# Kernel optimization log

Hardware: AMD Instinct MI355X
Metric: run time of the kernel (lower is better)

Reference implementation:

```python
import jax, jax.numpy as jnp
import numpy as np

SAMPLE_RATE = 4096.0  # matches init_kwargs sample_rate
STATE_DIM = 64
LENGTH, CHANNELS = 8192, 512


def setup_inputs() -> dict:
    key = jax.random.key(0)
    kx, kc = jax.random.split(key)
    x = jax.random.normal(kx, (LENGTH, CHANNELS), dtype=jnp.float32)
    # param init exactly as in the flax module
    logA = jnp.log(1.0 + jnp.arange(STATE_DIM, dtype=jnp.float32))
    B = jnp.ones((STATE_DIM,), dtype=jnp.float32)
    C = 0.01 * jax.random.normal(kc, (STATE_DIM,), dtype=jnp.float32)  # nn.initializers.normal() stddev=0.01
    return {"x": x, "logA": logA, "B": B, "C": C}


def reference(x, logA, B, C):
    # ZOH-style discretization: A = -exp(logA); Abar = exp(A*dt); Bbar = (Abar-1)*B/A
    dt = 1.0 / SAMPLE_RATE
    A = -jnp.exp(logA)                # (N,)
    Abar = jnp.exp(A * dt)            # (N,)
    Bbar = (Abar - 1.0) * B / A       # (N,)

    channels = x.shape[1]
    h0 = jnp.zeros((channels, logA.shape[0]), dtype=x.dtype)  # (C, N)

    def step(h, xt):
        # h: (C, N), xt: (C,)
        h = Abar[None, :] * h + xt[:, None] * Bbar[None, :]
        y = h @ C                      # (C,)
        return h, y

    _, y = jax.lax.scan(step, h0, x)   # y: (L, C)
    return y
```

## Files before the change

### kernel.cpp

```cpp
#include <hip/hip_runtime.h>
#include <math.h>

#define LENGTH   8192
#define CHANNELS 512
#define NSTATE   64
#define TCHUNK   64
#define NCHUNK   (LENGTH / TCHUNK)
#define E_ELEMS  (NCHUNK * NSTATE * CHANNELS)

__global__ void k_setup(const float* __restrict__ logA, const float* __restrict__ B,
                        const float* __restrict__ C, float* __restrict__ cons) {
    int n = threadIdx.x;
    if (n < NSTATE) {
        double A    = -exp((double)logA[n]);
        double ab   = exp(A * (1.0 / 4096.0));
        double Bbar = (ab - 1.0) * (double)B[n] / A;
        double abT  = ab;
        #pragma unroll
        for (int i = 0; i < 6; ++i) abT *= abT;
        cons[n]              = (float)ab;
        cons[NSTATE + n]     = (float)((double)C[n] * Bbar);
        cons[2 * NSTATE + n] = (float)abT;
    }
}

#define PF1 8
__global__ __launch_bounds__(256, 1) void k_pass1(const float* __restrict__ x,
                                                  const float* __restrict__ cons,
                                                  float* __restrict__ E) {
    int gtid = blockIdx.x * 256 + threadIdx.x;
    int c = gtid & (CHANNELS - 1);
    int k = gtid >> 9;
    const float* xp = x + (size_t)k * TCHUNK * CHANNELS + c;

    float h[NSTATE];
    #pragma unroll
    for (int n = 0; n < NSTATE; ++n) h[n] = 0.f;

    float xbuf[PF1];
    #pragma unroll
    for (int j = 0; j < PF1; ++j) xbuf[j] = xp[(size_t)j * CHANNELS];

    #pragma unroll 1
    for (int t0 = 0; t0 < TCHUNK; t0 += PF1) {
        #pragma unroll
        for (int j = 0; j < PF1; ++j) {
            int nt = t0 + PF1 + j;
            if (nt > TCHUNK - 1) nt = TCHUNK - 1;
            float xn = xp[(size_t)nt * CHANNELS];
            float xv = xbuf[j];
            #pragma unroll
            for (int n = 0; n < NSTATE; ++n) h[n] = fmaf(cons[n], h[n], xv);
            xbuf[j] = xn;
        }
    }

    float* Ep = E + (size_t)k * NSTATE * CHANNELS + c;
    #pragma unroll
    for (int n = 0; n < NSTATE; ++n) Ep[(size_t)n * CHANNELS] = h[n];
}

#define G2 16
__global__ __launch_bounds__(64, 1) void k_pass2(float* __restrict__ W,
                                                 const float* __restrict__ cons) {
    int gtid = blockIdx.x * 64 + threadIdx.x;
    int c = gtid & (CHANNELS - 1);
    int n = gtid >> 9;
    float aT = cons[2 * NSTATE + n];
    float* p = W + (size_t)n * CHANNELS + c;
    const size_t S = (size_t)NSTATE * CHANNELS;

    float e[2][G2];
    #pragma unroll
    for (int j = 0; j < G2; ++j) e[0][j] = p[(size_t)j * S];

    float hc = 0.f;
    #pragma unroll
    for (int k0 = 0; k0 < NCHUNK; k0 += G2) {
        const int cur = (k0 / G2) & 1;
        const int nxt = cur ^ 1;
        if (k0 + G2 < NCHUNK) {
            #pragma unroll
            for (int j = 0; j < G2; ++j) e[nxt][j] = p[(size_t)(k0 + G2 + j) * S];
        }
        #pragma unroll
        for (int j = 0; j < G2; ++j) {
            p[(size_t)(k0 + j) * S] = hc;
            hc = fmaf(aT, hc, e[cur][j]);
        }
    }
}

#define PF3 4
__global__ __launch_bounds__(256, 1) void k_pass3(const float* __restrict__ x,
                                                  const float* __restrict__ cons,
                                                  const float* __restrict__ Wc,
                                                  float* __restrict__ y) {
    int gtid = blockIdx.x * 256 + threadIdx.x;
    int c = gtid & (CHANNELS - 1);
    int k = gtid >> 9;

    const float* cp = Wc + (size_t)k * NSTATE * CHANNELS + c;
    float h[NSTATE];
    #pragma unroll
    for (int n = 0; n < NSTATE; ++n) h[n] = cp[(size_t)n * CHANNELS];

    const float* xp = x + (size_t)k * TCHUNK * CHANNELS + c;
    float*       yp = y + (size_t)k * TCHUNK * CHANNELS + c;

    float xbuf[PF3];
    #pragma unroll
    for (int j = 0; j < PF3; ++j) xbuf[j] = xp[(size_t)j * CHANNELS];

    #pragma unroll 1
    for (int t0 = 0; t0 < TCHUNK; t0 += PF3) {
        #pragma unroll
        for (int j = 0; j < PF3; ++j) {
            int nt = t0 + PF3 + j;
            if (nt > TCHUNK - 1) nt = TCHUNK - 1;
            float xn = xp[(size_t)nt * CHANNELS];
            float xv = xbuf[j];
            float y0 = 0.f, y1 = 0.f, y2 = 0.f, y3 = 0.f;
            #pragma unroll
            for (int n = 0; n < NSTATE; n += 4) {
                h[n]     = fmaf(cons[n],     h[n],     xv);
                h[n + 1] = fmaf(cons[n + 1], h[n + 1], xv);
                h[n + 2] = fmaf(cons[n + 2], h[n + 2], xv);
                h[n + 3] = fmaf(cons[n + 3], h[n + 3], xv);
                y0 = fmaf(cons[NSTATE + n],     h[n],     y0);
                y1 = fmaf(cons[NSTATE + n + 1], h[n + 1], y1);
                y2 = fmaf(cons[NSTATE + n + 2], h[n + 2], y2);
                y3 = fmaf(cons[NSTATE + n + 3], h[n + 3], y3);
            }
            yp[(size_t)(t0 + j) * CHANNELS] = (y0 + y1) + (y2 + y3);
            xbuf[j] = xn;
        }
    }
}

__global__ __launch_bounds__(256) void k_fallback(const float* __restrict__ x,
                                                  const float* __restrict__ logA,
                                                  const float* __restrict__ B,
                                                  const float* __restrict__ C,
                                                  float* __restrict__ y) {
    int c = blockIdx.x * blockDim.x + threadIdx.x;
    if (c >= CHANNELS) return;
    float Abar[NSTATE], CB[NSTATE], h[NSTATE];
    for (int n = 0; n < NSTATE; ++n) {
        double A    = -exp((double)logA[n]);
        double ab   = exp(A * (1.0 / 4096.0));
        double Bbar = (ab - 1.0) * (double)B[n] / A;
        Abar[n] = (float)ab;
        CB[n]   = (float)((double)C[n] * Bbar);
        h[n]    = 0.f;
    }
    for (int t = 0; t < LENGTH; ++t) {
        float xv = x[(size_t)t * CHANNELS + c];
        float acc = 0.f;
        for (int n = 0; n < NSTATE; ++n) {
            h[n] = fmaf(Abar[n], h[n], xv);
            acc  = fmaf(CB[n], h[n], acc);
        }
        y[(size_t)t * CHANNELS + c] = acc;
    }
}

extern "C" void kernel_launch(void* const* d_in, const int* in_sizes, int n_in,
                              void* d_out, int out_size, void* d_ws, size_t ws_size,
                              hipStream_t stream) {
    const float* x    = (const float*)d_in[0];
    const float* logA = (const float*)d_in[1];
    const float* B    = (const float*)d_in[2];
    const float* C    = (const float*)d_in[3];
    float* yout = (float*)d_out;

    size_t need = (size_t)(E_ELEMS + 3 * NSTATE) * sizeof(float);
    if (ws_size < need) {
        k_fallback<<<(CHANNELS + 255) / 256, 256, 0, stream>>>(x, logA, B, C, yout);
        return;
    }

    float* W    = (float*)d_ws;
    float* cons = W + E_ELEMS;

    k_setup<<<1, 64, 0, stream>>>(logA, B, C, cons);
    k_pass1<<<(NCHUNK * CHANNELS) / 256, 256, 0, stream>>>(x, cons, W);
    k_pass2<<<(NSTATE * CHANNELS) / 64, 64, 0, stream>>>(W, cons);
    k_pass3<<<(NCHUNK * CHANNELS) / 256, 256, 0, stream>>>(x, cons, W, yout);
}
```

Baseline: 115.3 us.

## Reformulate chunk passes as matrix products with precomputed decay and Toeplitz tables

The per-chunk recurrences in pass1 and pass3 are replaced by dense matmul-like accumulations. They use precomputed decay-power (G), Toeplitz impulse-response (T) and output-projection (P) tables built in the setup kernel, with input tiles staged through LDS. This removes the serial per-timestep dependency chain and the low-occupancy one-thread-per-channel-chunk design, and gives more blocks and independent FMAs. In exchange it does more arithmetic per output and changes floating-point summation order.

```diff
diff --git a/kernel.cpp b/kernel.cpp
--- a/kernel.cpp
+++ b/kernel.cpp
@@ -8,56 +8,85 @@
 #define NCHUNK   (LENGTH / TCHUNK)
 #define E_ELEMS  (NCHUNK * NSTATE * CHANNELS)
 
+
 __global__ void k_setup(const float* __restrict__ logA, const float* __restrict__ B,
-                        const float* __restrict__ C, float* __restrict__ cons) {
+                        const float* __restrict__ C, float* __restrict__ cons,
+                        float* __restrict__ Gt, float* __restrict__ Tt,
+                        float* __restrict__ Pt) {
+    __shared__ double contrib[64][65];
+    __shared__ double Kd[64];
     int n = threadIdx.x;
-    if (n < NSTATE) {
-        double A    = -exp((double)logA[n]);
-        double ab   = exp(A * (1.0 / 4096.0));
-        double Bbar = (ab - 1.0) * (double)B[n] / A;
-        double abT  = ab;
-        #pragma unroll
-        for (int i = 0; i < 6; ++i) abT *= abT;
-        cons[n]              = (float)ab;
-        cons[NSTATE + n]     = (float)((double)C[n] * Bbar);
-        cons[2 * NSTATE + n] = (float)abT;
-    }
-}
-
-#define PF1 8
-__global__ __launch_bounds__(256, 1) void k_pass1(const float* __restrict__ x,
-                                                  const float* __restrict__ cons,
+
+    double A    = -exp((double)logA[n]);
+    double ab   = exp(A * (1.0 / 4096.0));
+    double Bbar = (ab - 1.0) * (double)B[n] / A;
+    double CB   = (double)C[n] * Bbar;
+
+    cons[n]       = (float)ab;
+    cons[64 + n]  = (float)CB;
+    cons[128 + n] = (float)exp(A * (64.0 / 4096.0));
+
+    double p = 1.0;
+    #pragma unroll 1
+    for (int e = 0; e < 64; ++e) { Gt[(63 - e) * 64 + n] = (float)p; p *= ab; }
+
+    p = ab;
+    #pragma unroll 1
+    for (int t = 0; t < 64; ++t) { Pt[n * 64 + t] = (float)(CB * p); p *= ab; }
+
+    p = CB;
+    #pragma unroll 1
+    for (int d = 0; d < 64; ++d) { contrib[n][d] = p; p *= ab; }
+    __syncthreads();
+
+    double Ksum = 0.0;
+    #pragma unroll 1
+    for (int m = 0; m < 64; ++m) Ksum += contrib[m][n];
+    Kd[n] = Ksum;
+    __syncthreads();
+
+    int s = n;
+    #pragma unroll 1
+    for (int t = 0; t < 64; ++t) Tt[s * 64 + t] = (t >= s) ? (float)Kd[t - s] : 0.f;
+}
+
+__global__ __launch_bounds__(256, 4) void k_pass1(const float* __restrict__ x,
+                                                  const float* __restrict__ Gt,
                                                   float* __restrict__ E) {
-    int gtid = blockIdx.x * 256 + threadIdx.x;
-    int c = gtid & (CHANNELS - 1);
-    int k = gtid >> 9;
-    const float* xp = x + (size_t)k * TCHUNK * CHANNELS + c;
-
-    float h[NSTATE];
-    #pragma unroll
-    for (int n = 0; n < NSTATE; ++n) h[n] = 0.f;
-
-    float xbuf[PF1];
-    #pragma unroll
-    for (int j = 0; j < PF1; ++j) xbuf[j] = xp[(size_t)j * CHANNELS];
-
-    #pragma unroll 1
-    for (int t0 = 0; t0 < TCHUNK; t0 += PF1) {
-        #pragma unroll
-        for (int j = 0; j < PF1; ++j) {
-            int nt = t0 + PF1 + j;
-            if (nt > TCHUNK - 1) nt = TCHUNK - 1;
-            float xn = xp[(size_t)nt * CHANNELS];
-            float xv = xbuf[j];
-            #pragma unroll
-            for (int n = 0; n < NSTATE; ++n) h[n] = fmaf(cons[n], h[n], xv);
-            xbuf[j] = xn;
-        }
-    }
-
-    float* Ep = E + (size_t)k * NSTATE * CHANNELS + c;
-    #pragma unroll
-    for (int n = 0; n < NSTATE; ++n) Ep[(size_t)n * CHANNELS] = h[n];
+    __shared__ float Xl[64 * 64];
+    int tid = threadIdx.x;
+    int k   = blockIdx.x >> 3;
+    int c0  = (blockIdx.x & 7) * 64;
+
+    const float* xsrc = x + (size_t)k * TCHUNK * CHANNELS + c0;
+    #pragma unroll
+    for (int i = 0; i < 4; ++i) {
+        int idx = tid + 256 * i;
+        int s   = idx >> 4;
+        int cq  = (idx & 15) * 4;
+        *(float4*)&Xl[s * 64 + cq] = *(const float4*)(xsrc + (size_t)s * CHANNELS + cq);
+    }
+    __syncthreads();
+
+    int w    = __builtin_amdgcn_readfirstlane(tid >> 6);
+    int lane = tid & 63;
+    const float* Gw = Gt + 16 * w;
+
+    float acc[16];
+    #pragma unroll
+    for (int j = 0; j < 16; ++j) acc[j] = 0.f;
+
+    #pragma unroll 4
+    for (int s = 0; s < 64; ++s) {
+        float xv = Xl[s * 64 + lane];
+        const float* g = Gw + s * 64;
+        #pragma unroll
+        for (int j = 0; j < 16; ++j) acc[j] = fmaf(g[j], xv, acc[j]);
+    }
+
+    float* Ep = E + ((size_t)k * NSTATE + 16 * w) * CHANNELS + c0 + lane;
+    #pragma unroll
+    for (int j = 0; j < 16; ++j) Ep[(size_t)j * CHANNELS] = acc[j];
 }
 
 #define G2 16
@@ -66,7 +95,7 @@
     int gtid = blockIdx.x * 64 + threadIdx.x;
     int c = gtid & (CHANNELS - 1);
     int n = gtid >> 9;
-    float aT = cons[2 * NSTATE + n];
+    float aT = cons[128 + n];
     float* p = W + (size_t)n * CHANNELS + c;
     const size_t S = (size_t)NSTATE * CHANNELS;
 
@@ -91,51 +120,58 @@
     }
 }
 
-#define PF3 4
-__global__ __launch_bounds__(256, 1) void k_pass3(const float* __restrict__ x,
-                                                  const float* __restrict__ cons,
+__global__ __launch_bounds__(256, 4) void k_pass3(const float* __restrict__ x,
+                                                  const float* __restrict__ Tt,
+                                                  const float* __restrict__ Pt,
                                                   const float* __restrict__ Wc,
                                                   float* __restrict__ y) {
-    int gtid = blockIdx.x * 256 + threadIdx.x;
-    int c = gtid & (CHANNELS - 1);
-    int k = gtid >> 9;
-
-    const float* cp = Wc + (size_t)k * NSTATE * CHANNELS + c;
-    float h[NSTATE];
-    #pragma unroll
-    for (int n = 0; n < NSTATE; ++n) h[n] = cp[(size_t)n * CHANNELS];
-
-    const float* xp = x + (size_t)k * TCHUNK * CHANNELS + c;
-    float*       yp = y + (size_t)k * TCHUNK * CHANNELS + c;
-
-    float xbuf[PF3];
-    #pragma unroll
-    for (int j = 0; j < PF3; ++j) xbuf[j] = xp[(size_t)j * CHANNELS];
-
-    #pragma unroll 1
-    for (int t0 = 0; t0 < TCHUNK; t0 += PF3) {
-        #pragma unroll
-        for (int j = 0; j < PF3; ++j) {
-            int nt = t0 + PF3 + j;
-            if (nt > TCHUNK - 1) nt = TCHUNK - 1;
-            float xn = xp[(size_t)nt * CHANNELS];
-            float xv = xbuf[j];
-            float y0 = 0.f, y1 = 0.f, y2 = 0.f, y3 = 0.f;
-            #pragma unroll
-            for (int n = 0; n < NSTATE; n += 4) {
-                h[n]     = fmaf(cons[n],     h[n],     xv);
-                h[n + 1] = fmaf(cons[n + 1], h[n + 1], xv);
-                h[n + 2] = fmaf(cons[n + 2], h[n + 2], xv);
-                h[n + 3] = fmaf(cons[n + 3], h[n + 3], xv);
-                y0 = fmaf(cons[NSTATE + n],     h[n],     y0);
-                y1 = fmaf(cons[NSTATE + n + 1], h[n + 1], y1);
-                y2 = fmaf(cons[NSTATE + n + 2], h[n + 2], y2);
-                y3 = fmaf(cons[NSTATE + n + 3], h[n + 3], y3);
-            }
-            yp[(size_t)(t0 + j) * CHANNELS] = (y0 + y1) + (y2 + y3);
-            xbuf[j] = xn;
-        }
-    }
+    __shared__ float Xl[64 * 64];
+    __shared__ float Hl[64 * 64];
+    int tid = threadIdx.x;
+    int k   = blockIdx.x >> 3;
+    int c0  = (blockIdx.x & 7) * 64;
+
+    const float* xsrc = x  + (size_t)k * TCHUNK * CHANNELS + c0;
+    const float* hsrc = Wc + (size_t)k * NSTATE * CHANNELS + c0;
+    #pragma unroll
+    for (int i = 0; i < 4; ++i) {
+        int idx = tid + 256 * i;
+        int s   = idx >> 4;
+        int cq  = (idx & 15) * 4;
+        *(float4*)&Xl[s * 64 + cq] = *(const float4*)(xsrc + (size_t)s * CHANNELS + cq);
+        *(float4*)&Hl[s * 64 + cq] = *(const float4*)(hsrc + (size_t)s * CHANNELS + cq);
+    }
+    __syncthreads();
+
+    int w    = __builtin_amdgcn_readfirstlane(tid >> 6);
+    int lane = tid & 63;
+    int t0   = 16 * w;
+
+    float acc[16];
+    #pragma unroll
+    for (int j = 0; j < 16; ++j) acc[j] = 0.f;
+
+    const float* Tw = Tt + t0;
+    #pragma unroll 4
+    for (int s = 0; s < 64; ++s) {
+        float xv = Xl[s * 64 + lane];
+        const float* tt = Tw + s * 64;
+        #pragma unroll
+        for (int j = 0; j < 16; ++j) acc[j] = fmaf(tt[j], xv, acc[j]);
+    }
+
+    const float* Pw = Pt + t0;
+    #pragma unroll 4
+    for (int n = 0; n < 64; ++n) {
+        float hv = Hl[n * 64 + lane];
+        const float* pp = Pw + n * 64;
+        #pragma unroll
+        for (int j = 0; j < 16; ++j) acc[j] = fmaf(pp[j], hv, acc[j]);
+    }
+
+    float* yp = y + ((size_t)k * TCHUNK + t0) * CHANNELS + c0 + lane;
+    #pragma unroll
+    for (int j = 0; j < 16; ++j) yp[(size_t)j * CHANNELS] = acc[j];
 }
 
 __global__ __launch_bounds__(256) void k_fallback(const float* __restrict__ x,
@@ -174,7 +210,7 @@
     const float* C    = (const float*)d_in[3];
     float* yout = (float*)d_out;
 
-    size_t need = (size_t)(E_ELEMS + 3 * NSTATE) * sizeof(float);
+    size_t need = (size_t)(E_ELEMS + 192 + 3 * 4096) * sizeof(float);
     if (ws_size < need) {
         k_fallback<<<(CHANNELS + 255) / 256, 256, 0, stream>>>(x, logA, B, C, yout);
         return;
@@ -182,9 +218,12 @@
 
     float* W    = (float*)d_ws;
     float* cons = W + E_ELEMS;
-
-    k_setup<<<1, 64, 0, stream>>>(logA, B, C, cons);
-    k_pass1<<<(NCHUNK * CHANNELS) / 256, 256, 0, stream>>>(x, cons, W);
+    float* Gt   = cons + 192;
+    float* Tt   = Gt + 4096;
+    float* Pt   = Tt + 4096;
+
+    k_setup<<<1, 64, 0, stream>>>(logA, B, C, cons, Gt, Tt, Pt);
+    k_pass1<<<NCHUNK * 8, 256, 0, stream>>>(x, Gt, W);
     k_pass2<<<(NSTATE * CHANNELS) / 64, 64, 0, stream>>>(W, cons);
-    k_pass3<<<(NCHUNK * CHANNELS) / 256, 256, 0, stream>>>(x, cons, W, yout);
-}
+    k_pass3<<<NCHUNK * 8, 256, 0, stream>>>(x, Tt, Pt, W, yout);
+}
```

After: 113.9 us. About the same (-1.2%).

## Recast chunked SSM scan passes as bf16x3 MFMA matrix products

Applied to the files above, without the earlier changes.

Pass 1 and pass 3 no longer run a sequential per-channel recurrence over 64 states. They become matrix products on the MFMA units. Pass 1 multiplies a decay matrix by each x tile to get the chunk-end state. Pass 3 combines a Toeplitz kernel matrix applied to x with a state-propagation matrix applied to the carried-in state to produce y. fp32 accuracy is approximated with hi/lo bf16 splitting (three products per pair), and the matrices are precomputed in a prep kernel. This cuts the per-thread serial FMA chains, but it adds shared-memory staging, and precision could fall below pure fp32.

```diff
diff --git a/kernel.cpp b/kernel.cpp
--- a/kernel.cpp
+++ b/kernel.cpp
@@ -7,66 +7,132 @@
 #define TCHUNK   64
 #define NCHUNK   (LENGTH / TCHUNK)
 #define E_ELEMS  (NCHUNK * NSTATE * CHANNELS)
-
-__global__ void k_setup(const float* __restrict__ logA, const float* __restrict__ B,
-                        const float* __restrict__ C, float* __restrict__ cons) {
-    int n = threadIdx.x;
-    if (n < NSTATE) {
-        double A    = -exp((double)logA[n]);
-        double ab   = exp(A * (1.0 / 4096.0));
-        double Bbar = (ab - 1.0) * (double)B[n] / A;
-        double abT  = ab;
-        #pragma unroll
-        for (int i = 0; i < 6; ++i) abT *= abT;
-        cons[n]              = (float)ab;
-        cons[NSTATE + n]     = (float)((double)C[n] * Bbar);
-        cons[2 * NSTATE + n] = (float)abT;
-    }
-}
-
-#define PF1 8
-__global__ __launch_bounds__(256, 1) void k_pass1(const float* __restrict__ x,
-                                                  const float* __restrict__ cons,
+#define TSTRIDE  72
+
+
+typedef __attribute__((ext_vector_type(8))) short bf16x8;
+typedef __attribute__((ext_vector_type(4))) float f32x4;
+
+static __device__ __forceinline__ unsigned short f2bf(float f) {
+    unsigned int u = __float_as_uint(f);
+    u += 0x7fff + ((u >> 16) & 1);
+    return (unsigned short)(u >> 16);
+}
+static __device__ __forceinline__ float bf2f(unsigned short h) {
+    return __uint_as_float(((unsigned int)h) << 16);
+}
+
+__global__ void k_prep(const float* __restrict__ logA, const float* __restrict__ B,
+                       const float* __restrict__ C, unsigned short* __restrict__ mats) {
+    __shared__ double dl2[64], dCB[64], Kp[256], Kd[64];
+    int tid = threadIdx.x;
+    if (tid < 64) {
+        double A    = -exp((double)logA[tid]);
+        double lab  = A * (1.0 / 4096.0);
+        double Bbar = expm1(lab) * (double)B[tid] / A;
+        dl2[tid] = lab;
+        dCB[tid] = (double)C[tid] * Bbar;
+    }
+    __syncthreads();
+    {
+        int d = tid & 63, q = tid >> 6;
+        double s = 0.0;
+        for (int i = 0; i < 16; ++i) { int n = q * 16 + i; s += dCB[n] * exp(dl2[n] * (double)d); }
+        Kp[q * 64 + d] = s;
+    }
+    __syncthreads();
+    if (tid < 64) Kd[tid] = (Kp[tid] + Kp[64 + tid]) + (Kp[128 + tid] + Kp[192 + tid]);
+    __syncthreads();
+
+    unsigned short *Gh = mats,          *Gl = mats + 4096;
+    unsigned short *Th = mats + 8192,   *Tl = mats + 12288;
+    unsigned short *Ph = mats + 16384,  *Pl = mats + 20480;
+    int r = tid >> 2, cb = (tid & 3) * 16;
+    for (int j = 0; j < 16; ++j) {
+        int kk = cb + j;
+        double g = exp(dl2[r] * (double)(63 - kk));
+        unsigned short h = f2bf((float)g);
+        Gh[r * 64 + kk] = h; Gl[r * 64 + kk] = f2bf((float)g - bf2f(h));
+
+        double tv = (r >= kk) ? Kd[r - kk] : 0.0;
+        h = f2bf((float)tv);
+        Th[r * 64 + kk] = h; Tl[r * 64 + kk] = f2bf((float)tv - bf2f(h));
+
+        double pv = dCB[kk] * exp(dl2[kk] * (double)(r + 1));
+        h = f2bf((float)pv);
+        Ph[r * 64 + kk] = h; Pl[r * 64 + kk] = f2bf((float)pv - bf2f(h));
+    }
+}
+
+static __device__ __forceinline__ void stage_tile(const float* __restrict__ src,
+                                                  unsigned short* __restrict__ Dh,
+                                                  unsigned short* __restrict__ Dl,
+                                                  int tid) {
+    int c = tid & 63, g = tid >> 6;
+    const float* sp = src + (size_t)(16 * g) * CHANNELS + c;
+    float v[16];
+    #pragma unroll
+    for (int j = 0; j < 16; ++j) v[j] = sp[(size_t)j * CHANNELS];
+    bf16x8 h0, h1, l0, l1;
+    #pragma unroll
+    for (int j = 0; j < 8; ++j) {
+        unsigned short a = f2bf(v[j]), b = f2bf(v[8 + j]);
+        h0[j] = (short)a; h1[j] = (short)b;
+        l0[j] = (short)f2bf(v[j] - bf2f(a));
+        l1[j] = (short)f2bf(v[8 + j] - bf2f(b));
+    }
+    *(bf16x8*)&Dh[c * TSTRIDE + 16 * g]     = h0;
+    *(bf16x8*)&Dh[c * TSTRIDE + 16 * g + 8] = h1;
+    *(bf16x8*)&Dl[c * TSTRIDE + 16 * g]     = l0;
+    *(bf16x8*)&Dl[c * TSTRIDE + 16 * g + 8] = l1;
+}
+
+__global__ __launch_bounds__(256, 4) void k_pass1(const float* __restrict__ x,
+                                                  const unsigned short* __restrict__ mats,
                                                   float* __restrict__ E) {
-    int gtid = blockIdx.x * 256 + threadIdx.x;
-    int c = gtid & (CHANNELS - 1);
-    int k = gtid >> 9;
-    const float* xp = x + (size_t)k * TCHUNK * CHANNELS + c;
-
-    float h[NSTATE];
-    #pragma unroll
-    for (int n = 0; n < NSTATE; ++n) h[n] = 0.f;
-
-    float xbuf[PF1];
-    #pragma unroll
-    for (int j = 0; j < PF1; ++j) xbuf[j] = xp[(size_t)j * CHANNELS];
-
-    #pragma unroll 1
-    for (int t0 = 0; t0 < TCHUNK; t0 += PF1) {
-        #pragma unroll
-        for (int j = 0; j < PF1; ++j) {
-            int nt = t0 + PF1 + j;
-            if (nt > TCHUNK - 1) nt = TCHUNK - 1;
-            float xn = xp[(size_t)nt * CHANNELS];
-            float xv = xbuf[j];
-            #pragma unroll
-            for (int n = 0; n < NSTATE; ++n) h[n] = fmaf(cons[n], h[n], xv);
-            xbuf[j] = xn;
-        }
-    }
-
-    float* Ep = E + (size_t)k * NSTATE * CHANNELS + c;
-    #pragma unroll
-    for (int n = 0; n < NSTATE; ++n) Ep[(size_t)n * CHANNELS] = h[n];
+    __shared__ unsigned short Xh[64 * TSTRIDE], Xl[64 * TSTRIDE];
+    int tid = threadIdx.x;
+    int k = blockIdx.x >> 3, c0g = (blockIdx.x & 7) * 64;
+
+    stage_tile(x + (size_t)k * TCHUNK * CHANNELS + c0g, Xh, Xl, tid);
+    __syncthreads();
+
+    int w = tid >> 6, lane = tid & 63;
+    int p = lane & 15, q = lane >> 4;
+    const unsigned short *Gh = mats, *Gl = mats + 4096;
+
+    f32x4 acc[4] = {{0.f,0.f,0.f,0.f},{0.f,0.f,0.f,0.f},{0.f,0.f,0.f,0.f},{0.f,0.f,0.f,0.f}};
+    #pragma unroll
+    for (int ks = 0; ks < 2; ++ks) {
+        int bidx = (16 * w + p) * TSTRIDE + 32 * ks + 8 * q;
+        bf16x8 bh = *(bf16x8*)&Xh[bidx];
+        bf16x8 bl = *(bf16x8*)&Xl[bidx];
+        #pragma unroll
+        for (int mt = 0; mt < 4; ++mt) {
+            int aidx = (16 * mt + p) * 64 + 32 * ks + 8 * q;
+            bf16x8 ah = *(const bf16x8*)&Gh[aidx];
+            bf16x8 al = *(const bf16x8*)&Gl[aidx];
+            acc[mt] = __builtin_amdgcn_mfma_f32_16x16x32_bf16(ah, bh, acc[mt], 0, 0, 0);
+            acc[mt] = __builtin_amdgcn_mfma_f32_16x16x32_bf16(ah, bl, acc[mt], 0, 0, 0);
+            acc[mt] = __builtin_amdgcn_mfma_f32_16x16x32_bf16(al, bh, acc[mt], 0, 0, 0);
+        }
+    }
+    #pragma unroll
+    for (int mt = 0; mt < 4; ++mt) {
+        float* Ep = E + ((size_t)k * NSTATE + 16 * mt + 4 * q) * CHANNELS + c0g + 16 * w + p;
+        #pragma unroll
+        for (int r = 0; r < 4; ++r) Ep[(size_t)r * CHANNELS] = acc[mt][r];
+    }
 }
 
 #define G2 16
 __global__ __launch_bounds__(64, 1) void k_pass2(float* __restrict__ W,
-                                                 const float* __restrict__ cons) {
+                                                 const float* __restrict__ logA) {
     int gtid = blockIdx.x * 64 + threadIdx.x;
     int c = gtid & (CHANNELS - 1);
     int n = gtid >> 9;
-    float aT = cons[2 * NSTATE + n];
+    float A  = -expf(logA[n]);
+    float aT = expf(A * (64.0f / 4096.0f));
     float* p = W + (size_t)n * CHANNELS + c;
     const size_t S = (size_t)NSTATE * CHANNELS;
 
@@ -77,8 +143,7 @@
     float hc = 0.f;
     #pragma unroll
     for (int k0 = 0; k0 < NCHUNK; k0 += G2) {
-        const int cur = (k0 / G2) & 1;
-        const int nxt = cur ^ 1;
+        const int cur = (k0 / G2) & 1, nxt = cur ^ 1;
         if (k0 + G2 < NCHUNK) {
             #pragma unroll
             for (int j = 0; j < G2; ++j) e[nxt][j] = p[(size_t)(k0 + G2 + j) * S];
@@ -91,50 +156,52 @@
     }
 }
 
-#define PF3 4
-__global__ __launch_bounds__(256, 1) void k_pass3(const float* __restrict__ x,
-                                                  const float* __restrict__ cons,
+__global__ __launch_bounds__(256, 4) void k_pass3(const float* __restrict__ x,
+                                                  const unsigned short* __restrict__ mats,
                                                   const float* __restrict__ Wc,
                                                   float* __restrict__ y) {
-    int gtid = blockIdx.x * 256 + threadIdx.x;
-    int c = gtid & (CHANNELS - 1);
-    int k = gtid >> 9;
-
-    const float* cp = Wc + (size_t)k * NSTATE * CHANNELS + c;
-    float h[NSTATE];
-    #pragma unroll
-    for (int n = 0; n < NSTATE; ++n) h[n] = cp[(size_t)n * CHANNELS];
-
-    const float* xp = x + (size_t)k * TCHUNK * CHANNELS + c;
-    float*       yp = y + (size_t)k * TCHUNK * CHANNELS + c;
-
-    float xbuf[PF3];
-    #pragma unroll
-    for (int j = 0; j < PF3; ++j) xbuf[j] = xp[(size_t)j * CHANNELS];
-
-    #pragma unroll 1
-    for (int t0 = 0; t0 < TCHUNK; t0 += PF3) {
-        #pragma unroll
-        for (int j = 0; j < PF3; ++j) {
-            int nt = t0 + PF3 + j;
-            if (nt > TCHUNK - 1) nt = TCHUNK - 1;
-            float xn = xp[(size_t)nt * CHANNELS];
-            float xv = xbuf[j];
-            float y0 = 0.f, y1 = 0.f, y2 = 0.f, y3 = 0.f;
-            #pragma unroll
-            for (int n = 0; n < NSTATE; n += 4) {
-                h[n]     = fmaf(cons[n],     h[n],     xv);
-                h[n + 1] = fmaf(cons[n + 1], h[n + 1], xv);
-                h[n + 2] = fmaf(cons[n + 2], h[n + 2], xv);
-                h[n + 3] = fmaf(cons[n + 3], h[n + 3], xv);
-                y0 = fmaf(cons[NSTATE + n],     h[n],     y0);
-                y1 = fmaf(cons[NSTATE + n + 1], h[n + 1], y1);
-                y2 = fmaf(cons[NSTATE + n + 2], h[n + 2], y2);
-                y3 = fmaf(cons[NSTATE + n + 3], h[n + 3], y3);
-            }
-            yp[(size_t)(t0 + j) * CHANNELS] = (y0 + y1) + (y2 + y3);
-            xbuf[j] = xn;
-        }
+    __shared__ unsigned short Xh[64 * TSTRIDE], Xl[64 * TSTRIDE];
+    __shared__ unsigned short Hh[64 * TSTRIDE], Hl[64 * TSTRIDE];
+    int tid = threadIdx.x;
+    int k = blockIdx.x >> 3, c0g = (blockIdx.x & 7) * 64;
+
+    stage_tile(x  + (size_t)k * TCHUNK * CHANNELS + c0g, Xh, Xl, tid);
+    stage_tile(Wc + (size_t)k * NSTATE * CHANNELS + c0g, Hh, Hl, tid);
+    __syncthreads();
+
+    int w = tid >> 6, lane = tid & 63;
+    int p = lane & 15, q = lane >> 4;
+    const unsigned short *Th = mats + 8192,  *Tl = mats + 12288;
+    const unsigned short *Ph = mats + 16384, *Pl = mats + 20480;
+
+    f32x4 acc[4] = {{0.f,0.f,0.f,0.f},{0.f,0.f,0.f,0.f},{0.f,0.f,0.f,0.f},{0.f,0.f,0.f,0.f}};
+    #pragma unroll
+    for (int ks = 0; ks < 2; ++ks) {
+        int bidx = (16 * w + p) * TSTRIDE + 32 * ks + 8 * q;
+        bf16x8 bxh = *(bf16x8*)&Xh[bidx];
+        bf16x8 bxl = *(bf16x8*)&Xl[bidx];
+        bf16x8 bhh = *(bf16x8*)&Hh[bidx];
+        bf16x8 bhl = *(bf16x8*)&Hl[bidx];
+        #pragma unroll
+        for (int mt = 0; mt < 4; ++mt) {
+            int aidx = (16 * mt + p) * 64 + 32 * ks + 8 * q;
+            bf16x8 ath = *(const bf16x8*)&Th[aidx];
+            bf16x8 atl = *(const bf16x8*)&Tl[aidx];
+            acc[mt] = __builtin_amdgcn_mfma_f32_16x16x32_bf16(ath, bxh, acc[mt], 0, 0, 0);
+            acc[mt] = __builtin_amdgcn_mfma_f32_16x16x32_bf16(ath, bxl, acc[mt], 0, 0, 0);
+            acc[mt] = __builtin_amdgcn_mfma_f32_16x16x32_bf16(atl, bxh, acc[mt], 0, 0, 0);
+            bf16x8 aph = *(const bf16x8*)&Ph[aidx];
+            bf16x8 apl = *(const bf16x8*)&Pl[aidx];
+            acc[mt] = __builtin_amdgcn_mfma_f32_16x16x32_bf16(aph, bhh, acc[mt], 0, 0, 0);
+            acc[mt] = __builtin_amdgcn_mfma_f32_16x16x32_bf16(aph, bhl, acc[mt], 0, 0, 0);
+            acc[mt] = __builtin_amdgcn_mfma_f32_16x16x32_bf16(apl, bhh, acc[mt], 0, 0, 0);
+        }
+    }
+    #pragma unroll
+    for (int mt = 0; mt < 4; ++mt) {
+        float* yp = y + ((size_t)k * TCHUNK + 16 * mt + 4 * q) * CHANNELS + c0g + 16 * w + p;
+        #pragma unroll
+        for (int r = 0; r < 4; ++r) yp[(size_t)r * CHANNELS] = acc[mt][r];
     }
 }
 
@@ -147,12 +214,10 @@
     if (c >= CHANNELS) return;
     float Abar[NSTATE], CB[NSTATE], h[NSTATE];
     for (int n = 0; n < NSTATE; ++n) {
-        double A    = -exp((double)logA[n]);
-        double ab   = exp(A * (1.0 / 4096.0));
-        double Bbar = (ab - 1.0) * (double)B[n] / A;
-        Abar[n] = (float)ab;
-        CB[n]   = (float)((double)C[n] * Bbar);
-        h[n]    = 0.f;
+        float A    = -expf(logA[n]);
+        float ab   = expf(A / 4096.0f);
+        float Bbar = expm1f(A / 4096.0f) * B[n] / A;
+        Abar[n] = ab; CB[n] = C[n] * Bbar; h[n] = 0.f;
     }
     for (int t = 0; t < LENGTH; ++t) {
         float xv = x[(size_t)t * CHANNELS + c];
@@ -174,17 +239,16 @@
     const float* C    = (const float*)d_in[3];
     float* yout = (float*)d_out;
 
-    size_t need = (size_t)(E_ELEMS + 3 * NSTATE) * sizeof(float);
+    size_t need = (size_t)E_ELEMS * sizeof(float) + 6 * 4096 * sizeof(unsigned short);
     if (ws_size < need) {
         k_fallback<<<(CHANNELS + 255) / 256, 256, 0, stream>>>(x, logA, B, C, yout);
         return;
     }
-
-    float* W    = (float*)d_ws;
-    float* cons = W + E_ELEMS;
-
-    k_setup<<<1, 64, 0, stream>>>(logA, B, C, cons);
-    k_pass1<<<(NCHUNK * CHANNELS) / 256, 256, 0, stream>>>(x, cons, W);
-    k_pass2<<<(NSTATE * CHANNELS) / 64, 64, 0, stream>>>(W, cons);
-    k_pass3<<<(NCHUNK * CHANNELS) / 256, 256, 0, stream>>>(x, cons, W, yout);
-}
+    float*          W    = (float*)d_ws;
+    unsigned short* mats = (unsigned short*)(W + E_ELEMS);
+
+    k_prep <<<1, 256, 0, stream>>>(logA, B, C, mats);
+    k_pass1<<<NCHUNK * 8, 256, 0, stream>>>(x, mats, W);
+    k_pass2<<<(NSTATE * CHANNELS) / 64, 64, 0, stream>>>(W, logA);
+    k_pass3<<<NCHUNK * 8, 256, 0, stream>>>(x, mats, W, yout);
+}
```

Result: slower. 120.5 us (+4.5%).
